# Optimization experiments

Hardware: AMD Instinct MI355X
Metric: run time of the kernel (lower is better)

## Reference

```python
import jax, jax.numpy as jnp
import numpy as np

T, B = 4096, 8192


def setup_inputs() -> dict:
    key = jax.random.key(0)
    k1, k2 = jax.random.split(key)
    # binary Bernoulli(0.5) observations, shape [T, B, 1]
    inputs = jnp.round(jax.random.uniform(k1, (T, B, 1), dtype=jnp.float32))
    # decay_rate = exp(-1 / 10**loglifetime), loglifetime ~ U(0.5, 2.5)
    loglifetime = jax.random.uniform(k2, (), minval=0.5, maxval=2.5)
    decay_rate = jnp.exp(-1.0 / (10.0 ** loglifetime)).astype(jnp.float32)
    return {"inputs": inputs, "decay_rate": decay_rate}


def _forward(inputs, decay_rate):
    # order == 1 ('transition' estimate): bigram leaky counts
    x = inputs[:, :, 0]                      # [T, B]
    n_seqs = x.shape[1]
    z = jnp.zeros((n_seqs,), dtype=inputs.dtype)
    d = decay_rate

    def step(carry, x_t):
        n10, n11, na0, na1, prev = carry
        n10 = d * (n10 + x_t * (1.0 - prev))   # ones after a 0
        n11 = d * (n11 + x_t * prev)           # ones after a 1
        na0 = d * (na0 + (1.0 - prev))         # all after a 0
        na1 = d * (na1 + prev)                 # all after a 1
        return (n10, n11, na0, na1, x_t), (n10, n11, na0, na1)

    _, (n10s, n11s, na0s, na1s) = jax.lax.scan(step, (z, z, z, z, z), x)

    N_ONES_PRIOR, N_ALL_PRIOR = 1.0, 2.0
    p0 = (n10s + N_ONES_PRIOR) / (na0s + N_ALL_PRIOR)   # [T, B]
    p1 = (n11s + N_ONES_PRIOR) / (na1s + N_ALL_PRIOR)   # [T, B]
    # prediction conditioned on current observation
    pred = p0 * (1.0 - x) + p1 * x                      # [T, B]
    return pred[:, :, None]                             # [T, B, 1]


def reference(inputs, decay_rate):
    return _forward(inputs, decay_rate)
```

## Files before the change

### kernel.cpp

```cpp
#include <hip/hip_runtime.h>


constexpr int T_DIM  = 4096;
constexpr int B_DIM  = 8192;
constexpr int NCHUNK = 64;
constexpr int CLEN   = T_DIM / NCHUNK;
constexpr int VEC    = 2;
constexpr int UNROLL = 8;

typedef float v2f __attribute__((ext_vector_type(2)));
typedef unsigned long long u64;


__global__ __launch_bounds__(256) void partial_kernel(
    const float* __restrict__ x, const float* __restrict__ dptr,
    float* __restrict__ ws)
{
    const float d  = *dptr;
    const int   c  = blockIdx.y;
    const int   b0 = (blockIdx.x * blockDim.x + threadIdx.x) * VEC;
    const long  t0 = (long)c * CLEN;

    float prev[VEC];
    if (c == 0) {
        prev[0] = prev[1] = 0.0f;
    } else {
        const float2 pv = *reinterpret_cast<const float2*>(x + (t0 - 1) * B_DIM + b0);
        prev[0] = pv.x; prev[1] = pv.y;
    }

    float n10[VEC] = {0,0}, n11[VEC] = {0,0}, na0[VEC] = {0,0}, na1[VEC] = {0,0};
    u64 mask[VEC] = {0ull, 0ull};

    const float* p = x + t0 * B_DIM + b0;
    for (int kk = 0; kk < CLEN; kk += UNROLL) {
        float2 xv[UNROLL];
        #pragma unroll
        for (int u = 0; u < UNROLL; ++u)
            xv[u] = *reinterpret_cast<const float2*>(p + (size_t)u * B_DIM);
        p += (size_t)UNROLL * B_DIM;
        #pragma unroll
        for (int u = 0; u < UNROLL; ++u) {
            const int   k = kk + u;
            const float xs[VEC] = {xv[u].x, xv[u].y};
            #pragma unroll
            for (int j = 0; j < VEC; ++j) {
                const float xt = xs[j];
                mask[j] |= (u64)(unsigned)xt << k;
                const float pr = prev[j];
                const float om = 1.0f - pr;
                n10[j] = d * (n10[j] + xt * om);
                n11[j] = d * (n11[j] + xt * pr);
                na0[j] = d * (na0[j] + om);
                na1[j] = d * (na1[j] + pr);
                prev[j] = xt;
            }
        }
    }

    float* w = ws + (size_t)c * B_DIM + b0;
    *reinterpret_cast<float2*>(w + (size_t)0 * NCHUNK * B_DIM) = make_float2(n10[0], n10[1]);
    *reinterpret_cast<float2*>(w + (size_t)1 * NCHUNK * B_DIM) = make_float2(n11[0], n11[1]);
    *reinterpret_cast<float2*>(w + (size_t)2 * NCHUNK * B_DIM) = make_float2(na0[0], na0[1]);
    *reinterpret_cast<float2*>(w + (size_t)3 * NCHUNK * B_DIM) = make_float2(na1[0], na1[1]);

    u64* bits = reinterpret_cast<u64*>(ws + (size_t)4 * NCHUNK * B_DIM);
    bits[(size_t)c * B_DIM + b0]     = mask[0];
    bits[(size_t)c * B_DIM + b0 + 1] = mask[1];
}

__global__ __launch_bounds__(256) void scan_kernel(
    const float* __restrict__ dptr, float* __restrict__ ws)
{
    float dL = *dptr;
    #pragma unroll
    for (int i = 0; i < 6; ++i) dL = dL * dL;

    const int tid = blockIdx.x * blockDim.x + threadIdx.x;
    float* p = ws + (size_t)(tid >> 13) * NCHUNK * B_DIM + (tid & (B_DIM - 1));

    float l[NCHUNK];
    #pragma unroll
    for (int c = 0; c < NCHUNK; ++c) l[c] = p[(size_t)c * B_DIM];

    float s = 0.f;
    #pragma unroll
    for (int c = 0; c < NCHUNK; ++c) {
        p[(size_t)c * B_DIM] = s;
        s = dL * s + l[c];
    }
}

__global__ __launch_bounds__(256) void final_kernel(
    const float* __restrict__ dptr, const float* __restrict__ ws,
    float* __restrict__ out)
{
    const float d  = *dptr;
    const int   c  = blockIdx.y;
    const int   b0 = (blockIdx.x * blockDim.x + threadIdx.x) * VEC;

    const float* w = ws + (size_t)c * B_DIM + b0;
    const float2 s0 = *reinterpret_cast<const float2*>(w + (size_t)0 * NCHUNK * B_DIM);
    const float2 s1 = *reinterpret_cast<const float2*>(w + (size_t)1 * NCHUNK * B_DIM);
    const float2 s2 = *reinterpret_cast<const float2*>(w + (size_t)2 * NCHUNK * B_DIM);
    const float2 s3 = *reinterpret_cast<const float2*>(w + (size_t)3 * NCHUNK * B_DIM);
    float n10[VEC] = {s0.x, s0.y};
    float n11[VEC] = {s1.x, s1.y};
    float na0[VEC] = {s2.x, s2.y};
    float na1[VEC] = {s3.x, s3.y};

    const u64* bits = reinterpret_cast<const u64*>(ws + (size_t)4 * NCHUNK * B_DIM);
    u64 mask[VEC];
    mask[0] = bits[(size_t)c * B_DIM + b0];
    mask[1] = bits[(size_t)c * B_DIM + b0 + 1];

    float prev[VEC];
    if (c == 0) {
        prev[0] = prev[1] = 0.0f;
    } else {
        const u64 pm0 = bits[(size_t)(c - 1) * B_DIM + b0];
        const u64 pm1 = bits[(size_t)(c - 1) * B_DIM + b0 + 1];
        prev[0] = (float)(unsigned)(pm0 >> 63);
        prev[1] = (float)(unsigned)(pm1 >> 63);
    }

    float* q = out + (size_t)c * CLEN * B_DIM + b0;
    for (int kk = 0; kk < CLEN; kk += UNROLL) {
        #pragma unroll
        for (int u = 0; u < UNROLL; ++u) {
            const int k = kk + u;
            float pr2[VEC];
            #pragma unroll
            for (int j = 0; j < VEC; ++j) {
                const float xt = (float)(unsigned)((mask[j] >> k) & 1ull);
                const float pv = prev[j];
                const float om = 1.0f - pv;
                n10[j] = d * (n10[j] + xt * om);
                n11[j] = d * (n11[j] + xt * pv);
                na0[j] = d * (na0[j] + om);
                na1[j] = d * (na1[j] + pv);
                prev[j] = xt;
                const float p0 = (n10[j] + 1.0f) * __builtin_amdgcn_rcpf(na0[j] + 2.0f);
                const float p1 = (n11[j] + 1.0f) * __builtin_amdgcn_rcpf(na1[j] + 2.0f);
                pr2[j] = p0 + (p1 - p0) * xt;
            }
            v2f ov; ov.x = pr2[0]; ov.y = pr2[1];
            __builtin_nontemporal_store(ov, reinterpret_cast<v2f*>(q + (size_t)u * B_DIM));
        }
        q += (size_t)UNROLL * B_DIM;
    }
}

extern "C" void kernel_launch(void* const* d_in, const int* in_sizes, int n_in,
                              void* d_out, int out_size, void* d_ws, size_t ws_size,
                              hipStream_t stream) {
    const float* x  = (const float*)d_in[0];
    const float* dr = (const float*)d_in[1];
    float* ws  = (float*)d_ws;
    float* out = (float*)d_out;

    dim3 blk(256);
    dim3 grid1(B_DIM / VEC / 256, NCHUNK);
    partial_kernel<<<grid1, blk, 0, stream>>>(x, dr, ws);
    scan_kernel<<<(4 * B_DIM) / 256, blk, 0, stream>>>(dr, ws);
    final_kernel<<<grid1, blk, 0, stream>>>(dr, ws, out);
}
```

Measured before the change: 241.0 us.

## Reduce tracked counters to two via algebraic identities, widen to float4 and double-buffer loads

Result: no change. 239.2 us (-0.7%).

```diff
diff --git a/kernel.cpp b/kernel.cpp
--- a/kernel.cpp
+++ b/kernel.cpp
@@ -5,12 +5,12 @@
 constexpr int B_DIM  = 8192;
 constexpr int NCHUNK = 64;
 constexpr int CLEN   = T_DIM / NCHUNK;
-constexpr int VEC    = 2;
+constexpr int VEC    = 4;
 constexpr int UNROLL = 8;
 
-typedef float v2f __attribute__((ext_vector_type(2)));
+typedef float v4f __attribute__((ext_vector_type(4)));
 typedef unsigned long long u64;
-
+typedef u64 v2u __attribute__((ext_vector_type(2)));
 
 __global__ __launch_bounds__(256) void partial_kernel(
     const float* __restrict__ x, const float* __restrict__ dptr,
@@ -23,50 +23,67 @@
 
     float prev[VEC];
     if (c == 0) {
-        prev[0] = prev[1] = 0.0f;
+        #pragma unroll
+        for (int j = 0; j < VEC; ++j) prev[j] = 0.0f;
     } else {
-        const float2 pv = *reinterpret_cast<const float2*>(x + (t0 - 1) * B_DIM + b0);
-        prev[0] = pv.x; prev[1] = pv.y;
+        const v4f pv = *reinterpret_cast<const v4f*>(x + (t0 - 1) * B_DIM + b0);
+        #pragma unroll
+        for (int j = 0; j < VEC; ++j) prev[j] = pv[j];
     }
 
-    float n10[VEC] = {0,0}, n11[VEC] = {0,0}, na0[VEC] = {0,0}, na1[VEC] = {0,0};
-    u64 mask[VEC] = {0ull, 0ull};
+    float m[VEC]   = {0.f, 0.f, 0.f, 0.f};
+    float n11[VEC] = {0.f, 0.f, 0.f, 0.f};
+    u64   mask[VEC] = {0ull, 0ull, 0ull, 0ull};
 
     const float* p = x + t0 * B_DIM + b0;
-    for (int kk = 0; kk < CLEN; kk += UNROLL) {
-        float2 xv[UNROLL];
-        #pragma unroll
-        for (int u = 0; u < UNROLL; ++u)
-            xv[u] = *reinterpret_cast<const float2*>(p + (size_t)u * B_DIM);
-        p += (size_t)UNROLL * B_DIM;
+
+    v4f A[UNROLL], Bv[UNROLL];
+    #pragma unroll
+    for (int u = 0; u < UNROLL; ++u)
+        A[u] = *reinterpret_cast<const v4f*>(p + (size_t)u * B_DIM);
+
+    auto compute = [&](const v4f* buf, int kbase) {
         #pragma unroll
         for (int u = 0; u < UNROLL; ++u) {
-            const int   k = kk + u;
-            const float xs[VEC] = {xv[u].x, xv[u].y};
+            const int k = kbase + u;
             #pragma unroll
             for (int j = 0; j < VEC; ++j) {
-                const float xt = xs[j];
+                const float xt = buf[u][j];
                 mask[j] |= (u64)(unsigned)xt << k;
-                const float pr = prev[j];
-                const float om = 1.0f - pr;
-                n10[j] = d * (n10[j] + xt * om);
-                n11[j] = d * (n11[j] + xt * pr);
-                na0[j] = d * (na0[j] + om);
-                na1[j] = d * (na1[j] + pr);
+                m[j]   = d * (m[j] + xt);
+                n11[j] = d * (n11[j] + xt * prev[j]);
                 prev[j] = xt;
             }
         }
+    };
+
+    #pragma unroll
+    for (int kk = 0; kk < CLEN; kk += 2 * UNROLL) {
+        #pragma unroll
+        for (int u = 0; u < UNROLL; ++u)
+            Bv[u] = *reinterpret_cast<const v4f*>(p + (size_t)(kk + UNROLL + u) * B_DIM);
+        compute(A, kk);
+        if (kk + 2 * UNROLL < CLEN) {
+            #pragma unroll
+            for (int u = 0; u < UNROLL; ++u)
+                A[u] = *reinterpret_cast<const v4f*>(p + (size_t)(kk + 2 * UNROLL + u) * B_DIM);
+        }
+        compute(Bv, kk + UNROLL);
     }
 
-    float* w = ws + (size_t)c * B_DIM + b0;
-    *reinterpret_cast<float2*>(w + (size_t)0 * NCHUNK * B_DIM) = make_float2(n10[0], n10[1]);
-    *reinterpret_cast<float2*>(w + (size_t)1 * NCHUNK * B_DIM) = make_float2(n11[0], n11[1]);
-    *reinterpret_cast<float2*>(w + (size_t)2 * NCHUNK * B_DIM) = make_float2(na0[0], na0[1]);
-    *reinterpret_cast<float2*>(w + (size_t)3 * NCHUNK * B_DIM) = make_float2(na1[0], na1[1]);
+    float* wm = ws + (size_t)c * B_DIM + b0;
+    v4f mv, nv;
+    #pragma unroll
+    for (int j = 0; j < VEC; ++j) { mv[j] = m[j]; nv[j] = n11[j]; }
+    *reinterpret_cast<v4f*>(wm)                                = mv;
+    *reinterpret_cast<v4f*>(wm + (size_t)NCHUNK * B_DIM)       = nv;
 
-    u64* bits = reinterpret_cast<u64*>(ws + (size_t)4 * NCHUNK * B_DIM);
-    bits[(size_t)c * B_DIM + b0]     = mask[0];
-    bits[(size_t)c * B_DIM + b0 + 1] = mask[1];
+    u64* bits = reinterpret_cast<u64*>(ws + (size_t)2 * NCHUNK * B_DIM);
+    v2u b01, b23;
+    b01[0] = mask[0]; b01[1] = mask[1];
+    b23[0] = mask[2]; b23[1] = mask[3];
+    *reinterpret_cast<v2u*>(&bits[(size_t)c * B_DIM + b0])     = b01;
+    *reinterpret_cast<v2u*>(&bits[(size_t)c * B_DIM + b0 + 2]) = b23;
 }
 
 __global__ __launch_bounds__(256) void scan_kernel(
@@ -95,33 +112,40 @@
     const float* __restrict__ dptr, const float* __restrict__ ws,
     float* __restrict__ out)
 {
-    const float d  = *dptr;
-    const int   c  = blockIdx.y;
-    const int   b0 = (blockIdx.x * blockDim.x + threadIdx.x) * VEC;
+    const float d = *dptr;
+    float dL = d;
+    #pragma unroll
+    for (int i = 0; i < 6; ++i) dL = dL * dL;
+
+    const int c  = blockIdx.y;
+    const int b0 = (blockIdx.x * blockDim.x + threadIdx.x) * VEC;
 
     const float* w = ws + (size_t)c * B_DIM + b0;
-    const float2 s0 = *reinterpret_cast<const float2*>(w + (size_t)0 * NCHUNK * B_DIM);
-    const float2 s1 = *reinterpret_cast<const float2*>(w + (size_t)1 * NCHUNK * B_DIM);
-    const float2 s2 = *reinterpret_cast<const float2*>(w + (size_t)2 * NCHUNK * B_DIM);
-    const float2 s3 = *reinterpret_cast<const float2*>(w + (size_t)3 * NCHUNK * B_DIM);
-    float n10[VEC] = {s0.x, s0.y};
-    float n11[VEC] = {s1.x, s1.y};
-    float na0[VEC] = {s2.x, s2.y};
-    float na1[VEC] = {s3.x, s3.y};
+    const v4f mi = *reinterpret_cast<const v4f*>(w);
+    const v4f ni = *reinterpret_cast<const v4f*>(w + (size_t)NCHUNK * B_DIM);
+    float m[VEC], n11[VEC];
+    #pragma unroll
+    for (int j = 0; j < VEC; ++j) { m[j] = mi[j]; n11[j] = ni[j]; }
 
-    const u64* bits = reinterpret_cast<const u64*>(ws + (size_t)4 * NCHUNK * B_DIM);
+    float dLc = 1.f, sq = dL;
+    int cc = c;
+    #pragma unroll
+    for (int i = 0; i < 6; ++i) { if (cc & 1) dLc *= sq; sq *= sq; cc >>= 1; }
+    float na = d * (1.f - dLc) / (1.f - d);
+
+    const u64* bits = reinterpret_cast<const u64*>(ws + (size_t)2 * NCHUNK * B_DIM);
     u64 mask[VEC];
-    mask[0] = bits[(size_t)c * B_DIM + b0];
-    mask[1] = bits[(size_t)c * B_DIM + b0 + 1];
+    #pragma unroll
+    for (int j = 0; j < VEC; ++j) mask[j] = bits[(size_t)c * B_DIM + b0 + j];
 
-    float prev[VEC];
+    bool pb[VEC];
     if (c == 0) {
-        prev[0] = prev[1] = 0.0f;
+        #pragma unroll
+        for (int j = 0; j < VEC; ++j) pb[j] = false;
     } else {
-        const u64 pm0 = bits[(size_t)(c - 1) * B_DIM + b0];
-        const u64 pm1 = bits[(size_t)(c - 1) * B_DIM + b0 + 1];
-        prev[0] = (float)(unsigned)(pm0 >> 63);
-        prev[1] = (float)(unsigned)(pm1 >> 63);
+        #pragma unroll
+        for (int j = 0; j < VEC; ++j)
+            pb[j] = (bits[(size_t)(c - 1) * B_DIM + b0 + j] >> 63) & 1ull;
     }
 
     float* q = out + (size_t)c * CLEN * B_DIM + b0;
@@ -129,23 +153,23 @@
         #pragma unroll
         for (int u = 0; u < UNROLL; ++u) {
             const int k = kk + u;
-            float pr2[VEC];
+            na = d * (na + 1.f);
+            float pr[VEC];
             #pragma unroll
             for (int j = 0; j < VEC; ++j) {
-                const float xt = (float)(unsigned)((mask[j] >> k) & 1ull);
-                const float pv = prev[j];
-                const float om = 1.0f - pv;
-                n10[j] = d * (n10[j] + xt * om);
-                n11[j] = d * (n11[j] + xt * pv);
-                na0[j] = d * (na0[j] + om);
-                na1[j] = d * (na1[j] + pv);
-                prev[j] = xt;
-                const float p0 = (n10[j] + 1.0f) * __builtin_amdgcn_rcpf(na0[j] + 2.0f);
-                const float p1 = (n11[j] + 1.0f) * __builtin_amdgcn_rcpf(na1[j] + 2.0f);
-                pr2[j] = p0 + (p1 - p0) * xt;
+                const bool  xb = (mask[j] >> k) & 1ull;
+                const float mo = m[j];
+                m[j]   = d * (mo + (xb ? 1.f : 0.f));
+                n11[j] = d * (n11[j] + ((xb && pb[j]) ? 1.f : 0.f));
+                const float num = xb ? (n11[j] + 1.f) : (m[j] - n11[j] + 1.f);
+                const float den = xb ? (mo + 2.f)     : (na - mo + 2.f);
+                pr[j] = num * __builtin_amdgcn_rcpf(den);
+                pb[j] = xb;
             }
-            v2f ov; ov.x = pr2[0]; ov.y = pr2[1];
-            __builtin_nontemporal_store(ov, reinterpret_cast<v2f*>(q + (size_t)u * B_DIM));
+            v4f ov;
+            #pragma unroll
+            for (int j = 0; j < VEC; ++j) ov[j] = pr[j];
+            __builtin_nontemporal_store(ov, reinterpret_cast<v4f*>(q + (size_t)u * B_DIM));
         }
         q += (size_t)UNROLL * B_DIM;
     }
@@ -162,6 +186,6 @@
     dim3 blk(256);
     dim3 grid1(B_DIM / VEC / 256, NCHUNK);
     partial_kernel<<<grid1, blk, 0, stream>>>(x, dr, ws);
-    scan_kernel<<<(4 * B_DIM) / 256, blk, 0, stream>>>(dr, ws);
+    scan_kernel<<<(2 * B_DIM) / 256, blk, 0, stream>>>(dr, ws);
     final_kernel<<<grid1, blk, 0, stream>>>(dr, ws, out);
 }
```
